# Performance work log

Measured on AMD Instinct MI355X. Metric: run time of the kernel, lower is better.

The kernel has to match this reference:

```python
import jax, jax.numpy as jnp
import numpy as np

DM, H, DK = 768, 12, 64

def setup_inputs() -> dict:
    key = jax.random.key(0)
    ks = jax.random.split(key, 12)
    B, S = 6, 1024
    sc = 1.0 / np.sqrt(DM)
    return {
        "Q": jax.random.normal(ks[0], (B, S, DM), jnp.float32),
        "K": jax.random.normal(ks[1], (B, S, DM), jnp.float32),
        "V": jax.random.normal(ks[2], (B, S, DM), jnp.float32),
        "attn_mask": jax.random.randint(ks[3], (B, S, S), 0, 2) > 0,
        "W_q": jax.random.uniform(ks[4], (DM, H * DK), jnp.float32, -sc, sc),
        "b_q": jax.random.uniform(ks[5], (H * DK,), jnp.float32, -sc, sc),
        "W_k": jax.random.uniform(ks[6], (DM, H * DK), jnp.float32, -sc, sc),
        "b_k": jax.random.uniform(ks[7], (H * DK,), jnp.float32, -sc, sc),
        "W_v": jax.random.uniform(ks[8], (DM, H * DK), jnp.float32, -sc, sc),
        "b_v": jax.random.uniform(ks[9], (H * DK,), jnp.float32, -sc, sc),
        "W_o": jax.random.uniform(ks[10], (H * DK, DM), jnp.float32, -1/np.sqrt(H*DK), 1/np.sqrt(H*DK)),
        "b_o": jax.random.uniform(ks[11], (DM,), jnp.float32, -1/np.sqrt(H*DK), 1/np.sqrt(H*DK)),
        "gamma": jnp.ones((DM,), jnp.float32),
        "beta": jnp.zeros((DM,), jnp.float32),
    }

def reference(Q, K, V, attn_mask, W_q, b_q, W_k, b_k, W_v, b_v, W_o, b_o, gamma, beta):
    B, S, _ = Q.shape
    residual = Q
    # projections -> [B, H, S, DK]
    q = (Q @ W_q + b_q).reshape(B, S, H, DK).transpose(0, 2, 1, 3)
    k = (K @ W_k + b_k).reshape(B, S, H, DK).transpose(0, 2, 1, 3)
    v = (V @ W_v + b_v).reshape(B, S, H, DK).transpose(0, 2, 1, 3)
    scores = jnp.einsum('bhqd,bhkd->bhqk', q, k) / np.sqrt(DK)
    scores = jnp.where(attn_mask[:, None, :, :], -1e9, scores)
    attn = jax.nn.softmax(scores, axis=-1)
    context = jnp.einsum('bhqk,bhkd->bhqd', attn, v)
    context = context.transpose(0, 2, 1, 3).reshape(B, S, H * DK)
    output = context @ W_o + b_o
    x = output + residual
    mu = jnp.mean(x, axis=-1, keepdims=True)
    var = jnp.var(x, axis=-1, keepdims=True)
    out = (x - mu) / jnp.sqrt(var + 1e-5) * gamma + beta
    return out, attn
```

## Files before the change

### kernel.cpp

```cpp
#include <hip/hip_runtime.h>
#include <hip/hip_bf16.h>

#define B 6
#define S 1024
#define H 12
#define DK 64
#define DM 768
#define M (B*S)
#define BH (B*H)

typedef __bf16 bf16;
typedef __attribute__((ext_vector_type(8))) __bf16 bf16x8;
typedef __attribute__((ext_vector_type(4))) float f32x4;

#define MFMA __builtin_amdgcn_mfma_f32_16x16x32_bf16

#define QSCALE 0.18033688011112042f

__device__ __forceinline__ float ex2(float x) {
  float r;
  asm("v_exp_f32 %0, %1" : "=v"(r) : "v"(x));
  return r;
}

__device__ __forceinline__ void lds_barrier() {
  asm volatile("s_waitcnt lgkmcnt(0)" ::: "memory");
  __builtin_amdgcn_s_barrier();
}

__device__ __forceinline__ bf16x8 cvt8(const float* p) {
  float4 u0 = *(const float4*)p;
  float4 u1 = *(const float4*)(p + 4);
  bf16x8 r;
  r[0]=(bf16)u0.x; r[1]=(bf16)u0.y; r[2]=(bf16)u0.z; r[3]=(bf16)u0.w;
  r[4]=(bf16)u1.x; r[5]=(bf16)u1.y; r[6]=(bf16)u1.z; r[7]=(bf16)u1.w;
  return r;
}

__global__ void k_prep(const float* __restrict__ Wq, const float* __restrict__ Wk,
                       const float* __restrict__ Wv, const float* __restrict__ Wo,
                       bf16* __restrict__ wt) {
  int zz = blockIdx.y;
  const float* W = zz==0?Wq : zz==1?Wk : zz==2?Wv : Wo;
  int idx = blockIdx.x*256 + threadIdx.x;
  int k = idx / DM, n = idx % DM;
  wt[(size_t)zz*DM*DM + (size_t)n*DM + k] = (bf16)W[idx];
}


__global__ __launch_bounds__(256, 3) void k_proj(
    const float* __restrict__ Qf, const float* __restrict__ Kf,
    const float* __restrict__ Vf, const bf16* __restrict__ wt,
    const float* __restrict__ bq, const float* __restrict__ bk,
    const float* __restrict__ bv,
    bf16* __restrict__ qb, bf16* __restrict__ kb, bf16* __restrict__ vt) {
  int z = blockIdx.z;
  const float* Xf   = z==0?Qf : z==1?Kf : Vf;
  const float* bias = z==0?bq : z==1?bk : bv;
  const bf16* Wt = wt + (size_t)z*DM*DM;
  int tid = threadIdx.x, lane = tid & 63, w = tid >> 6;
  int wr = w >> 1, wc = w & 1;
  int lr = lane & 15, lg = lane >> 4;
  int m0 = blockIdx.x*128;
  int n0 = blockIdx.y*128;

  __shared__ bf16 As[2][128*32];
  __shared__ bf16 Bs[2][128*32];

  const int srow = tid >> 1;
  const int c0   = (tid & 1) * 2;
  const int f    = (srow >> 1) & 3;
  const int sc   = (c0 ^ f) & ~1;
  const bool sw  = (f & 1);
  const float* asrc = Xf + (size_t)(m0 + srow)*DM + sc*8;
  const bf16*  bsrc = Wt + (size_t)(n0 + srow)*DM + sc*8;
  const int dst0 = srow*32 + c0*8;

  const int fs = (lr >> 1) & 3;
  const int fchunk = (lg ^ fs) * 8;

  f32x4 acc[4][4];
  #pragma unroll
  for (int i=0;i<4;++i)
    #pragma unroll
    for (int j=0;j<4;++j) acc[i][j] = (f32x4){0.f,0.f,0.f,0.f};

  {
    bf16x8 a0 = cvt8(asrc);
    bf16x8 a1 = cvt8(asrc + 8);
    bf16x8 b0 = *(const bf16x8*)(bsrc);
    bf16x8 b1 = *(const bf16x8*)(bsrc + 8);
    *(bf16x8*)&As[0][dst0]     = sw ? a1 : a0;
    *(bf16x8*)&As[0][dst0 + 8] = sw ? a0 : a1;
    *(bf16x8*)&Bs[0][dst0]     = sw ? b1 : b0;
    *(bf16x8*)&Bs[0][dst0 + 8] = sw ? b0 : b1;
  }
  lds_barrier();

  for (int t = 0; t < 24; ++t) {
    int cur = t & 1;
    bf16x8 pa0, pa1, pb0, pb1;
    if (t < 23) {
      int k0 = (t+1)*32;
      pa0 = cvt8(asrc + k0);
      pa1 = cvt8(asrc + k0 + 8);
      pb0 = *(const bf16x8*)(bsrc + k0);
      pb1 = *(const bf16x8*)(bsrc + k0 + 8);
    }
    bf16x8 af[4], bfr[4];
    #pragma unroll
    for (int mi=0;mi<4;++mi) af[mi]  = *(const bf16x8*)&As[cur][(wr*64 + mi*16 + lr)*32 + fchunk];
    #pragma unroll
    for (int ni=0;ni<4;++ni) bfr[ni] = *(const bf16x8*)&Bs[cur][(wc*64 + ni*16 + lr)*32 + fchunk];
    #pragma unroll
    for (int mi=0;mi<4;++mi)
      #pragma unroll
      for (int ni=0;ni<4;++ni)
        acc[mi][ni] = MFMA(af[mi], bfr[ni], acc[mi][ni], 0,0,0);
    if (t < 23) {
      *(bf16x8*)&As[cur^1][dst0]     = sw ? pa1 : pa0;
      *(bf16x8*)&As[cur^1][dst0 + 8] = sw ? pa0 : pa1;
      *(bf16x8*)&Bs[cur^1][dst0]     = sw ? pb1 : pb0;
      *(bf16x8*)&Bs[cur^1][dst0 + 8] = sw ? pb0 : pb1;
      lds_barrier();
    }
  }

  int mw = m0 + wr*64, nw = n0 + wc*64;
  #pragma unroll
  for (int ni=0;ni<4;++ni) {
    int n = nw + ni*16 + lr;
    float bs = bias[n];
    int h = n >> 6, d = n & 63;
    #pragma unroll
    for (int mi=0;mi<4;++mi)
      #pragma unroll
      for (int r=0;r<4;++r) {
        int m = mw + mi*16 + lg*4 + r;
        int bb = m >> 10, s = m & 1023;
        float val = acc[mi][ni][r] + bs;
        if (z == 0) {
          qb[((size_t)(bb*H + h)*S + s)*DK + d] = (bf16)(val * QSCALE);
        } else if (z == 1) {
          int dsw = ((((d>>3) ^ (s&7))) << 3) | (d&7);
          kb[((size_t)(bb*H + h)*S + s)*DK + dsw] = (bf16)val;
        } else {
          int ssw = (s & ~63) | ((((s&63)>>3) ^ (d&7)) << 3) | (s&7);
          vt[((size_t)(bb*H + h)*DK + d)*S + ssw] = (bf16)val;
        }
      }
  }
}

__global__ __launch_bounds__(256, 3) void k_oproj(
    const bf16* __restrict__ ctx, const bf16* __restrict__ wto,
    const float* __restrict__ bo, const float* __restrict__ res,
    float* __restrict__ x) {
  int tid = threadIdx.x, lane = tid & 63, w = tid >> 6;
  int wr = w >> 1, wc = w & 1;
  int lr = lane & 15, lg = lane >> 4;
  int m0 = blockIdx.x*128;
  int n0 = blockIdx.y*128;

  __shared__ bf16 As[2][128*32];
  __shared__ bf16 Bs[2][128*32];

  const int srow = tid >> 1;
  const int c0   = (tid & 1) * 2;
  const int f    = (srow >> 1) & 3;
  const int sc   = (c0 ^ f) & ~1;
  const bool sw  = (f & 1);
  const bf16* asrc = ctx + (size_t)(m0 + srow)*DM + sc*8;
  const bf16* bsrc = wto + (size_t)(n0 + srow)*DM + sc*8;
  const int dst0 = srow*32 + c0*8;
  const int fs = (lr >> 1) & 3;
  const int fchunk = (lg ^ fs) * 8;

  f32x4 acc[4][4];
  #pragma unroll
  for (int i=0;i<4;++i)
    #pragma unroll
    for (int j=0;j<4;++j) acc[i][j] = (f32x4){0.f,0.f,0.f,0.f};

  {
    bf16x8 a0 = *(const bf16x8*)(asrc);
    bf16x8 a1 = *(const bf16x8*)(asrc + 8);
    bf16x8 b0 = *(const bf16x8*)(bsrc);
    bf16x8 b1 = *(const bf16x8*)(bsrc + 8);
    *(bf16x8*)&As[0][dst0]     = sw ? a1 : a0;
    *(bf16x8*)&As[0][dst0 + 8] = sw ? a0 : a1;
    *(bf16x8*)&Bs[0][dst0]     = sw ? b1 : b0;
    *(bf16x8*)&Bs[0][dst0 + 8] = sw ? b0 : b1;
  }
  lds_barrier();

  for (int t = 0; t < 24; ++t) {
    int cur = t & 1;
    bf16x8 pa0, pa1, pb0, pb1;
    if (t < 23) {
      int k0 = (t+1)*32;
      pa0 = *(const bf16x8*)(asrc + k0);
      pa1 = *(const bf16x8*)(asrc + k0 + 8);
      pb0 = *(const bf16x8*)(bsrc + k0);
      pb1 = *(const bf16x8*)(bsrc + k0 + 8);
    }
    bf16x8 af[4], bfr[4];
    #pragma unroll
    for (int mi=0;mi<4;++mi) af[mi]  = *(const bf16x8*)&As[cur][(wr*64 + mi*16 + lr)*32 + fchunk];
    #pragma unroll
    for (int ni=0;ni<4;++ni) bfr[ni] = *(const bf16x8*)&Bs[cur][(wc*64 + ni*16 + lr)*32 + fchunk];
    #pragma unroll
    for (int mi=0;mi<4;++mi)
      #pragma unroll
      for (int ni=0;ni<4;++ni)
        acc[mi][ni] = MFMA(af[mi], bfr[ni], acc[mi][ni], 0,0,0);
    if (t < 23) {
      *(bf16x8*)&As[cur^1][dst0]     = sw ? pa1 : pa0;
      *(bf16x8*)&As[cur^1][dst0 + 8] = sw ? pa0 : pa1;
      *(bf16x8*)&Bs[cur^1][dst0]     = sw ? pb1 : pb0;
      *(bf16x8*)&Bs[cur^1][dst0 + 8] = sw ? pb0 : pb1;
      lds_barrier();
    }
  }

  int mw = m0 + wr*64, nw = n0 + wc*64;
  #pragma unroll
  for (int ni=0;ni<4;++ni) {
    int n = nw + ni*16 + lr;
    float bb = bo[n];
    #pragma unroll
    for (int mi=0;mi<4;++mi)
      #pragma unroll
      for (int r=0;r<4;++r) {
        int m = mw + mi*16 + lg*4 + r;
        x[(size_t)m*DM + n] = acc[mi][ni][r] + bb + res[(size_t)m*DM + n];
      }
  }
}

__device__ __forceinline__ unsigned pk2(float a, float b) {
  union { bf16 h[2]; unsigned u; } x;
  x.h[0] = (bf16)a; x.h[1] = (bf16)b;
  return x.u;
}

__global__ __launch_bounds__(256, 4) void k_fattn(
    const bf16* __restrict__ qb, const bf16* __restrict__ kb,
    const bf16* __restrict__ vt, const unsigned char* __restrict__ mask,
    float* __restrict__ attn, bf16* __restrict__ ctx) {
  int lin = blockIdx.x + 16*blockIdx.y;
  int xcd  = lin & 7;
  int slot = lin >> 3;
  int qt   = slot & 15;
  int bh   = xcd*9 + (slot >> 4);
  int b = bh / H, h = bh - b*H;
  int tid = threadIdx.x, lane = tid & 63, w = tid >> 6;
  int lr = lane & 15, lg = lane >> 4;
  int q0 = qt*64 + w*16;

  __shared__ bf16 Kb[2][4096];
  __shared__ bf16 Vb[2][4096];
  __shared__ bf16 pt[4][2][512];

  const bf16* qbase = qb + ((size_t)bh*S + q0 + lr)*DK + lg*8;
  bf16x8 qa0 = *(const bf16x8*)(qbase);
  bf16x8 qa1 = *(const bf16x8*)(qbase + 32);

  const char* kg = (const char*)(kb + (size_t)bh*S*DK);
  const char* vg = (const char*)(vt + (size_t)bh*DK*S);
  const unsigned char* mrow = mask + ((size_t)b*S + q0 + lr)*S;
  float* abase = attn + ((size_t)bh*S + q0 + lr)*S;

  const int koff0 = w*2048 + lane*16, koff1 = koff0 + 1024;
  const int kd0 = w*1024 + lane*8,    kd1 = kd0 + 512;
  const int vrow0 = w*16 + (lane>>3), vrow1 = vrow0 + 8;
  const int vcb = (lane&7)*16;
  const int vd0 = vrow0*64 + (lane&7)*8, vd1 = vd0 + 512;

  const int krow = lr*64;
  const int kf0o = krow + ((lg ^ (lr&7))<<3);
  const int kf1o = krow + (((4+lg) ^ (lr&7))<<3);
  const int swz  = (lr & 3) << 4;

  {
    bf16x8 a0 = *(const bf16x8*)(kg + koff0);
    bf16x8 a1 = *(const bf16x8*)(kg + koff1);
    *(bf16x8*)&Kb[0][kd0] = a0;
    *(bf16x8*)&Kb[0][kd1] = a1;
  }
  uchar4 mkn[4];
  #pragma unroll
  for (int i=0;i<4;++i) mkn[i] = *(const uchar4*)(mrow + i*16 + lg*4);
  lds_barrier();

  float sum = 0.f;
  for (int t = 0; t < 16; ++t) {
    int cur = t & 1;
    uchar4 mkc[4];
    #pragma unroll
    for (int i=0;i<4;++i) mkc[i] = mkn[i];
    bf16x8 kn0, kn1;
    if (t < 15) {
      kn0 = *(const bf16x8*)(kg + (t+1)*8192 + koff0);
      kn1 = *(const bf16x8*)(kg + (t+1)*8192 + koff1);
      #pragma unroll
      for (int i=0;i<4;++i) mkn[i] = *(const uchar4*)(mrow + (t+1)*64 + i*16 + lg*4);
    }
    #pragma unroll
    for (int i=0;i<4;++i) {
      bf16x8 kf0 = *(const bf16x8*)&Kb[cur][i*1024 + kf0o];
      bf16x8 kf1 = *(const bf16x8*)&Kb[cur][i*1024 + kf1o];
      f32x4 sc = {0.f,0.f,0.f,0.f};
      sc = MFMA(kf0, qa0, sc, 0,0,0);
      sc = MFMA(kf1, qa1, sc, 0,0,0);
      sum += mkc[i].x ? 0.f : ex2(sc[0]);
      sum += mkc[i].y ? 0.f : ex2(sc[1]);
      sum += mkc[i].z ? 0.f : ex2(sc[2]);
      sum += mkc[i].w ? 0.f : ex2(sc[3]);
    }
    if (t < 15) {
      *(bf16x8*)&Kb[cur^1][kd0] = kn0;
      *(bf16x8*)&Kb[cur^1][kd1] = kn1;
    }
    lds_barrier();
  }
  sum += __shfl_xor(sum, 16);
  sum += __shfl_xor(sum, 32);
  float inv = 1.f / sum;

  f32x4 cacc[4];
  #pragma unroll
  for (int d=0;d<4;++d) cacc[d] = (f32x4){0.f,0.f,0.f,0.f};

  {
    bf16x8 a0 = *(const bf16x8*)(kg + koff0);
    bf16x8 a1 = *(const bf16x8*)(kg + koff1);
    bf16x8 b0 = *(const bf16x8*)(vg + (size_t)vrow0*2048 + vcb);
    bf16x8 b1 = *(const bf16x8*)(vg + (size_t)vrow1*2048 + vcb);
    *(bf16x8*)&Kb[0][kd0] = a0;
    *(bf16x8*)&Kb[0][kd1] = a1;
    *(bf16x8*)&Vb[0][vd0] = b0;
    *(bf16x8*)&Vb[0][vd1] = b1;
    #pragma unroll
    for (int i=0;i<4;++i) mkn[i] = *(const uchar4*)(mrow + i*16 + lg*4);
  }
  lds_barrier();

  for (int t = 0; t < 16; ++t) {
    int cur = t & 1;
    uchar4 mkc[4];
    #pragma unroll
    for (int i=0;i<4;++i) mkc[i] = mkn[i];
    bf16x8 kn0, kn1, vn0, vn1;
    if (t < 15) {
      kn0 = *(const bf16x8*)(kg + (t+1)*8192 + koff0);
      kn1 = *(const bf16x8*)(kg + (t+1)*8192 + koff1);
      vn0 = *(const bf16x8*)(vg + (size_t)vrow0*2048 + (t+1)*128 + vcb);
      vn1 = *(const bf16x8*)(vg + (size_t)vrow1*2048 + (t+1)*128 + vcb);
      #pragma unroll
      for (int i=0;i<4;++i) mkn[i] = *(const uchar4*)(mrow + (t+1)*64 + i*16 + lg*4);
    }
    #pragma unroll
    for (int u = 0; u < 2; ++u) {
      char* buf = (char*)&pt[w][u][0];
      #pragma unroll
      for (int half = 0; half < 2; ++half) {
        int i = u*2 + half;
        bf16x8 kf0 = *(const bf16x8*)&Kb[cur][i*1024 + kf0o];
        bf16x8 kf1 = *(const bf16x8*)&Kb[cur][i*1024 + kf1o];
        f32x4 sc = {0.f,0.f,0.f,0.f};
        sc = MFMA(kf0, qa0, sc, 0,0,0);
        sc = MFMA(kf1, qa1, sc, 0,0,0);
        float p0 = mkc[i].x ? 0.f : ex2(sc[0])*inv;
        float p1 = mkc[i].y ? 0.f : ex2(sc[1])*inv;
        float p2 = mkc[i].z ? 0.f : ex2(sc[2])*inv;
        float p3 = mkc[i].w ? 0.f : ex2(sc[3])*inv;
        __builtin_nontemporal_store((f32x4){p0,p1,p2,p3},
                                    (f32x4*)(abase + t*64 + i*16 + lg*4));
        uint2 pw2; pw2.x = pk2(p0,p1); pw2.y = pk2(p2,p3);
        *(uint2*)(buf + lr*64 + ((half*32 + lg*8) ^ swz)) = pw2;
      }
      bf16x8 pa = *(const bf16x8*)(buf + lr*64 + ((lg*16) ^ swz));
      #pragma unroll
      for (int dd=0; dd<4; ++dd) {
        bf16x8 vf = *(const bf16x8*)&Vb[cur][dd*1024 + lr*64 + ((((u*4+lg) ^ (lr&7)))<<3)];
        cacc[dd] = MFMA(pa, vf, cacc[dd], 0,0,0);
      }
    }
    if (t < 15) {
      *(bf16x8*)&Kb[cur^1][kd0] = kn0;
      *(bf16x8*)&Kb[cur^1][kd1] = kn1;
      *(bf16x8*)&Vb[cur^1][vd0] = vn0;
      *(bf16x8*)&Vb[cur^1][vd1] = vn1;
    }
    lds_barrier();
  }

  #pragma unroll
  for (int d=0;d<4;++d)
    #pragma unroll
    for (int r=0;r<4;++r)
      ctx[((size_t)b*S + q0 + lg*4 + r)*DM + h*DK + d*16 + lr] = (bf16)cacc[d][r];
}

__global__ void k_ln(const float* __restrict__ x, const float* __restrict__ gamma,
                     const float* __restrict__ beta, float* __restrict__ out) {
  int row = blockIdx.x; int tid = threadIdx.x;
  const float* xr = x + (size_t)row*DM;
  float v0 = xr[tid], v1 = xr[tid+256], v2 = xr[tid+512];
  float s = v0+v1+v2, ss = v0*v0+v1*v1+v2*v2;
  #pragma unroll
  for (int off=32; off; off>>=1){ s += __shfl_xor(s,off); ss += __shfl_xor(ss,off); }
  __shared__ float sm[8];
  int w = tid>>6;
  if ((tid&63)==0){ sm[w]=s; sm[4+w]=ss; }
  __syncthreads();
  s = sm[0]+sm[1]+sm[2]+sm[3]; ss = sm[4]+sm[5]+sm[6]+sm[7];
  float mean = s * (1.f/DM);
  float var = ss * (1.f/DM) - mean*mean;
  float rstd = rsqrtf(var + 1e-5f);
  out[(size_t)row*DM + tid]     = (v0-mean)*rstd*gamma[tid]     + beta[tid];
  out[(size_t)row*DM + tid+256] = (v1-mean)*rstd*gamma[tid+256] + beta[tid+256];
  out[(size_t)row*DM + tid+512] = (v2-mean)*rstd*gamma[tid+512] + beta[tid+512];
}

extern "C" void kernel_launch(void* const* d_in, const int* in_sizes, int n_in,
                              void* d_out, int out_size, void* d_ws, size_t ws_size,
                              hipStream_t stream) {
  const float* Q  = (const float*)d_in[0];
  const float* K  = (const float*)d_in[1];
  const float* V  = (const float*)d_in[2];
  const unsigned char* mask = (const unsigned char*)d_in[3];
  const float* Wq = (const float*)d_in[4];
  const float* bq = (const float*)d_in[5];
  const float* Wk = (const float*)d_in[6];
  const float* bk = (const float*)d_in[7];
  const float* Wv = (const float*)d_in[8];
  const float* bv = (const float*)d_in[9];
  const float* Wo = (const float*)d_in[10];
  const float* bo = (const float*)d_in[11];
  const float* gamma = (const float*)d_in[12];
  const float* beta  = (const float*)d_in[13];

  char* ws = (char*)d_ws;
  bf16* wt  = (bf16*)(ws + 0);
  float* x  = (float*)(ws + 4718592);
  bf16* qb  = (bf16*)(ws + 33030144);
  bf16* kb  = (bf16*)(ws + 42467328);
  bf16* vt  = (bf16*)(ws + 51904512);
  bf16* ctx = (bf16*)(ws + 61341696);

  float* out  = (float*)d_out;
  float* attn = out + (size_t)B*S*DM;

  k_prep  <<<dim3(2304,4),  256, 0, stream>>>(Wq,Wk,Wv,Wo,wt);
  k_proj  <<<dim3(48,6,3),  256, 0, stream>>>(Q,K,V,wt,bq,bk,bv,qb,kb,vt);
  k_fattn <<<dim3(16,BH),   256, 0, stream>>>(qb,kb,vt,mask,attn,ctx);
  k_oproj <<<dim3(48,6),    256, 0, stream>>>(ctx, wt + (size_t)3*DM*DM, bo, Q, x);
  k_ln    <<<dim3(M),       256, 0, stream>>>(x,gamma,beta,out);
}
```

Baseline: 247.3 us.

## Load V fragments directly from global into registers, dropping the V LDS staging

The second attention pass no longer stages V tiles through double-buffered shared memory. Each lane now loads its MFMA B-operand fragments for V directly from global memory into registers, split into two register sets that are prefetched across the two halves of each 64-key tile. This removes the LDS writes and reads for V and halves the kernel's shared-memory footprint, which could raise occupancy. In exchange it adds more register pressure and uncoalesced, strided global loads, where each lane reads 16 bytes from a different V row, that must be hidden by the loop's prefetch distance.

```diff
diff --git a/kernel.cpp b/kernel.cpp
--- a/kernel.cpp
+++ b/kernel.cpp
@@ -259,7 +259,6 @@
   int q0 = qt*64 + w*16;
 
   __shared__ bf16 Kb[2][4096];
-  __shared__ bf16 Vb[2][4096];
   __shared__ bf16 pt[4][2][512];
 
   const bf16* qbase = qb + ((size_t)bh*S + q0 + lr)*DK + lg*8;
@@ -273,14 +272,18 @@
 
   const int koff0 = w*2048 + lane*16, koff1 = koff0 + 1024;
   const int kd0 = w*1024 + lane*8,    kd1 = kd0 + 512;
-  const int vrow0 = w*16 + (lane>>3), vrow1 = vrow0 + 8;
-  const int vcb = (lane&7)*16;
-  const int vd0 = vrow0*64 + (lane&7)*8, vd1 = vd0 + 512;
 
   const int krow = lr*64;
   const int kf0o = krow + ((lg ^ (lr&7))<<3);
   const int kf1o = krow + (((4+lg) ^ (lr&7))<<3);
   const int swz  = (lr & 3) << 4;
+
+  int voffA[4], voffB[4];
+  #pragma unroll
+  for (int dd=0;dd<4;++dd) {
+    voffA[dd] = (dd*16+lr)*2048 + (((lg)   ^ (lr&7)) << 4);
+    voffB[dd] = (dd*16+lr)*2048 + (((4+lg) ^ (lr&7)) << 4);
+  }
 
   {
     bf16x8 a0 = *(const bf16x8*)(kg + koff0);
@@ -332,15 +335,14 @@
   #pragma unroll
   for (int d=0;d<4;++d) cacc[d] = (f32x4){0.f,0.f,0.f,0.f};
 
+  bf16x8 VA[4], VB[4];
   {
     bf16x8 a0 = *(const bf16x8*)(kg + koff0);
     bf16x8 a1 = *(const bf16x8*)(kg + koff1);
-    bf16x8 b0 = *(const bf16x8*)(vg + (size_t)vrow0*2048 + vcb);
-    bf16x8 b1 = *(const bf16x8*)(vg + (size_t)vrow1*2048 + vcb);
     *(bf16x8*)&Kb[0][kd0] = a0;
     *(bf16x8*)&Kb[0][kd1] = a1;
-    *(bf16x8*)&Vb[0][vd0] = b0;
-    *(bf16x8*)&Vb[0][vd1] = b1;
+    #pragma unroll
+    for (int dd=0;dd<4;++dd) VA[dd] = *(const bf16x8*)(vg + voffA[dd]);
     #pragma unroll
     for (int i=0;i<4;++i) mkn[i] = *(const uchar4*)(mrow + i*16 + lg*4);
   }
@@ -351,21 +353,20 @@
     uchar4 mkc[4];
     #pragma unroll
     for (int i=0;i<4;++i) mkc[i] = mkn[i];
-    bf16x8 kn0, kn1, vn0, vn1;
+    bf16x8 kn0, kn1;
     if (t < 15) {
       kn0 = *(const bf16x8*)(kg + (t+1)*8192 + koff0);
       kn1 = *(const bf16x8*)(kg + (t+1)*8192 + koff1);
-      vn0 = *(const bf16x8*)(vg + (size_t)vrow0*2048 + (t+1)*128 + vcb);
-      vn1 = *(const bf16x8*)(vg + (size_t)vrow1*2048 + (t+1)*128 + vcb);
       #pragma unroll
       for (int i=0;i<4;++i) mkn[i] = *(const uchar4*)(mrow + (t+1)*64 + i*16 + lg*4);
     }
     #pragma unroll
-    for (int u = 0; u < 2; ++u) {
-      char* buf = (char*)&pt[w][u][0];
+    for (int dd=0;dd<4;++dd) VB[dd] = *(const bf16x8*)(vg + voffB[dd] + t*128);
+    {
+      char* buf = (char*)&pt[w][0][0];
       #pragma unroll
       for (int half = 0; half < 2; ++half) {
-        int i = u*2 + half;
+        int i = half;
         bf16x8 kf0 = *(const bf16x8*)&Kb[cur][i*1024 + kf0o];
         bf16x8 kf1 = *(const bf16x8*)&Kb[cur][i*1024 + kf1o];
         f32x4 sc = {0.f,0.f,0.f,0.f};
@@ -382,16 +383,40 @@
       }
       bf16x8 pa = *(const bf16x8*)(buf + lr*64 + ((lg*16) ^ swz));
       #pragma unroll
-      for (int dd=0; dd<4; ++dd) {
-        bf16x8 vf = *(const bf16x8*)&Vb[cur][dd*1024 + lr*64 + ((((u*4+lg) ^ (lr&7)))<<3)];
-        cacc[dd] = MFMA(pa, vf, cacc[dd], 0,0,0);
+      for (int dd=0; dd<4; ++dd)
+        cacc[dd] = MFMA(pa, VA[dd], cacc[dd], 0,0,0);
+    }
+    if (t < 15) {
+      #pragma unroll
+      for (int dd=0;dd<4;++dd) VA[dd] = *(const bf16x8*)(vg + voffA[dd] + (t+1)*128);
+    }
+    {
+      char* buf = (char*)&pt[w][1][0];
+      #pragma unroll
+      for (int half = 0; half < 2; ++half) {
+        int i = 2 + half;
+        bf16x8 kf0 = *(const bf16x8*)&Kb[cur][i*1024 + kf0o];
+        bf16x8 kf1 = *(const bf16x8*)&Kb[cur][i*1024 + kf1o];
+        f32x4 sc = {0.f,0.f,0.f,0.f};
+        sc = MFMA(kf0, qa0, sc, 0,0,0);
+        sc = MFMA(kf1, qa1, sc, 0,0,0);
+        float p0 = mkc[i].x ? 0.f : ex2(sc[0])*inv;
+        float p1 = mkc[i].y ? 0.f : ex2(sc[1])*inv;
+        float p2 = mkc[i].z ? 0.f : ex2(sc[2])*inv;
+        float p3 = mkc[i].w ? 0.f : ex2(sc[3])*inv;
+        __builtin_nontemporal_store((f32x4){p0,p1,p2,p3},
+                                    (f32x4*)(abase + t*64 + i*16 + lg*4));
+        uint2 pw2; pw2.x = pk2(p0,p1); pw2.y = pk2(p2,p3);
+        *(uint2*)(buf + lr*64 + ((half*32 + lg*8) ^ swz)) = pw2;
       }
+      bf16x8 pa = *(const bf16x8*)(buf + lr*64 + ((lg*16) ^ swz));
+      #pragma unroll
+      for (int dd=0; dd<4; ++dd)
+        cacc[dd] = MFMA(pa, VB[dd], cacc[dd], 0,0,0);
     }
     if (t < 15) {
       *(bf16x8*)&Kb[cur^1][kd0] = kn0;
       *(bf16x8*)&Kb[cur^1][kd1] = kn1;
-      *(bf16x8*)&Vb[cur^1][vd0] = vn0;
-      *(bf16x8*)&Vb[cur^1][vd1] = vn1;
     }
     lds_barrier();
   }
```

Result: no change. 249.8 us (+1.0%).
